# Optimization experiments

Hardware: AMD Instinct MI355X
Metric: run time of the kernel (lower is better)

Reference implementation:

```python
import jax, jax.numpy as jnp
import numpy as np

N = 100000       # n_entities + n_users
E = 1000000      # edges
D = 64           # entity_dim (phase/mod half-width)
R = 40           # n_relations
PI = 3.1415926235897933
GAMMA = 12.0
EMB_RANGE = (GAMMA + 2.0) / D   # (gamma + epsilon) / entity_dim
DIMS = [128, 64, 32, 16]        # conv_dim_list = [2*D] + [64,32,16]


def setup_inputs() -> dict:
    key = jax.random.key(0)
    ks = jax.random.split(key, 20)
    inp = {}
    inp["entity_embed"] = jax.random.uniform(ks[0], (N, 2 * D), minval=-EMB_RANGE, maxval=EMB_RANGE, dtype=jnp.float32)
    inp["rel_embed"] = jax.random.uniform(ks[1], (R, 3 * D), minval=-EMB_RANGE, maxval=EMB_RANGE, dtype=jnp.float32)
    inp["phase_w"] = jnp.array([[0.5 * EMB_RANGE]], dtype=jnp.float32)
    inp["mod_w"] = jnp.array([[1.0]], dtype=jnp.float32)
    names = [("W1_0", "b1_0", "W2_0", "b2_0"), ("W1_1", "b1_1", "W2_1", "b2_1"), ("W1_2", "b1_2", "W1_2b", "b2_2")]
    for i, (w1n, b1n, w2n, b2n) in enumerate(names):
        din, dout = DIMS[i], DIMS[i + 1]
        s = 1.0 / np.sqrt(din)
        inp[w1n] = jax.random.uniform(ks[2 + 4 * i], (dout, din), minval=-s, maxval=s, dtype=jnp.float32)
        inp[b1n] = jax.random.uniform(ks[3 + 4 * i], (dout,), minval=-s, maxval=s, dtype=jnp.float32)
        inp[w2n] = jax.random.uniform(ks[4 + 4 * i], (dout, din), minval=-s, maxval=s, dtype=jnp.float32)
        inp[b2n] = jax.random.uniform(ks[5 + 4 * i], (dout,), minval=-s, maxval=s, dtype=jnp.float32)
    inp["src"] = jax.random.randint(ks[14], (E,), 0, N, dtype=jnp.int32)
    inp["dst"] = jax.random.randint(ks[15], (E,), 0, N, dtype=jnp.int32)
    inp["etype"] = jax.random.randint(ks[16], (E,), 0, R, dtype=jnp.int32)
    return inp


def _edge_att(entity_embed, rel_embed, phase_w, mod_w, src, dst, etype):
    # HAKE att_score: h = dst node, t = src node (per original code)
    h = entity_embed[dst]            # [E, 2D]
    t = entity_embed[src]            # [E, 2D]
    r = rel_embed[etype]             # [E, 3D]
    scale = EMB_RANGE / PI
    ph, mh = h[:, :D], h[:, D:]
    pr, mr, br = r[:, :D], r[:, D:2 * D], r[:, 2 * D:]
    pt, mt = t[:, :D], t[:, D:]
    mr = jnp.abs(mr)
    br = jnp.minimum(br, 1.0)
    br = jnp.where(br < -mr, -mr, br)  # conditional write bias_relation[indicator] = -mod_relation
    mod_score = jnp.linalg.norm(mh * (mr + br) - mt * (1.0 - br), axis=1) * mod_w[0, 0]
    phase = (ph + pr - pt) / scale
    phase_score = jnp.sum(jnp.abs(jnp.sin(phase / 2.0)), axis=1) * phase_w[0, 0]
    att = phase_score + mod_score    # [E]
    # edge softmax over incoming edges of each dst node
    amax = jax.ops.segment_max(att, dst, num_segments=N)
    ex = jnp.exp(att - amax[dst])
    den = jax.ops.segment_sum(ex, dst, num_segments=N)
    return ex / den[dst]


def reference(entity_embed, rel_embed, phase_w, mod_w,
              W1_0, b1_0, W2_0, b2_0,
              W1_1, b1_1, W2_1, b2_1,
              W1_2, b1_2, W1_2b, b2_2,
              src, dst, etype):
    att = _edge_att(entity_embed, rel_embed, phase_w, mod_w, src, dst, etype)

    def layer(node, W1, b1, W2, b2):
        # u_mul_e('node','att','side') + sum('side','N_h')
        msg = node[src] * att[:, None]                    # [E, din]
        Nh = jax.ops.segment_sum(msg, dst, num_segments=N)
        # bi-interaction aggregator
        o = jax.nn.leaky_relu((node + Nh) @ W1.T + b1) + jax.nn.leaky_relu((node * Nh) @ W2.T + b2)
        nrm = jnp.linalg.norm(o, axis=1, keepdims=True)
        return o, o / jnp.maximum(nrm, 1e-12)             # (ego_embed, F.normalize)

    ego = entity_embed
    outs = [ego]
    for (W1, b1, W2, b2) in [(W1_0, b1_0, W2_0, b2_0), (W1_1, b1_1, W2_1, b2_1), (W1_2, b1_2, W1_2b, b2_2)]:
        ego, normed = layer(ego, W1, b1, W2, b2)
        outs.append(normed)
    return jnp.concatenate(outs, axis=1)                   # [N, 128+64+32+16]
```

## Files before the change

### kernel.cpp

```cpp
#include <hip/hip_runtime.h>
#include <math.h>


__global__ void hist_kernel(const int* __restrict__ dst, int* __restrict__ cnt,
                            int nedges) {
    int e = blockIdx.x * blockDim.x + threadIdx.x;
    if (e < nedges) atomicAdd(&cnt[dst[e]], 1);
}

__global__ __launch_bounds__(1024) void scan_block_kernel(
    const int* __restrict__ cnt, int* __restrict__ rowptr,
    int* __restrict__ bsum, int n) {
    __shared__ int swv[16];
    int tid = threadIdx.x, lane = tid & 63, wid = tid >> 6;
    int i = blockIdx.x * 1024 + tid;
    int v = (i < n) ? cnt[i] : 0;
    #pragma unroll
    for (int off = 1; off < 64; off <<= 1) {
        int t = __shfl_up(v, off, 64);
        if (lane >= off) v += t;
    }
    if (lane == 63) swv[wid] = v;
    __syncthreads();
    if (wid == 0) {
        int s = (lane < 16) ? swv[lane] : 0;
        #pragma unroll
        for (int off = 1; off < 16; off <<= 1) {
            int t = __shfl_up(s, off, 64);
            if (lane >= off) s += t;
        }
        if (lane < 16) swv[lane] = s;
    }
    __syncthreads();
    int offv = wid ? swv[wid - 1] : 0;
    if (i < n) rowptr[i + 1] = v + offv;
    if (tid == 1023) bsum[blockIdx.x] = v + offv;
}

__global__ __launch_bounds__(64) void scan_tops_kernel(
    const int* __restrict__ bsum, int* __restrict__ boff, int nb) {
    int l = threadIdx.x;
    int a = (2 * l < nb) ? bsum[2 * l] : 0;
    int b = (2 * l + 1 < nb) ? bsum[2 * l + 1] : 0;
    int s = a + b;
    #pragma unroll
    for (int off = 1; off < 64; off <<= 1) {
        int t = __shfl_up(s, off, 64);
        if (l >= off) s += t;
    }
    int excl = s - (a + b);
    if (2 * l < nb) boff[2 * l] = excl;
    if (2 * l + 1 < nb) boff[2 * l + 1] = excl + a;
}

__global__ __launch_bounds__(1024) void scan_add_kernel(
    int* __restrict__ rowptr, const int* __restrict__ boff, int n) {
    int i = blockIdx.x * 1024 + threadIdx.x;
    if (i < n) rowptr[i + 1] += boff[blockIdx.x];
    if (i == 0) rowptr[0] = 0;
}

__global__ void fill_kernel(const int* __restrict__ src, const int* __restrict__ dst,
                            const int* __restrict__ etype,
                            const int* __restrict__ rowptr, int* __restrict__ cursor,
                            int* __restrict__ se_s, int nedges) {
    int e = blockIdx.x * blockDim.x + threadIdx.x;
    if (e >= nedges) return;
    int d = dst[e];
    int slot = rowptr[d] + atomicAdd(&cursor[d], 1);
    se_s[slot] = src[e] | (etype[e] << 17);
}

__global__ void rel_prep_kernel(const float* __restrict__ rel,
                                float* __restrict__ relp, int nrel) {
    int i = blockIdx.x * blockDim.x + threadIdx.x;
    if (i >= nrel * 64) return;
    int r = i >> 6, d = i & 63;
    float pr = rel[r * 192 + d];
    float mr = fabsf(rel[r * 192 + 64 + d]);
    float br = rel[r * 192 + 128 + d];
    br = fminf(br, 1.0f);
    br = fmaxf(br, -mr);
    relp[r * 192 + d]       = mr + br;
    relp[r * 192 + 64 + d]  = 1.0f - br;
    relp[r * 192 + 128 + d] = pr;
}

__global__ __launch_bounds__(256) void att_gather_kernel(
    const float* __restrict__ embed, const float* __restrict__ relp,
    const float* __restrict__ pw, const float* __restrict__ mw,
    const int* __restrict__ se_s, const int* __restrict__ rowptr,
    float* __restrict__ att_s, float* __restrict__ ai,
    float* __restrict__ Nh, int nnodes)
{
    int v = blockIdx.x * 4 + (threadIdx.x >> 6);
    if (v >= nnodes) return;
    int lane = threadIdx.x & 63;
    int g = lane >> 3;
    int q = lane & 7;
    int beg = rowptr[v];
    int deg = rowptr[v + 1] - beg;

    const float K = (float)(0.5 * 3.1415926235897933 / 0.21875);
    float mwv = mw[0], pwv = pw[0];

    const float* hrow = embed + (size_t)v * 128;
    float4 hp0 = *(const float4*)(hrow + 8 * q);
    float4 hp1 = *(const float4*)(hrow + 8 * q + 4);
    float4 hm0 = *(const float4*)(hrow + 64 + 8 * q);
    float4 hm1 = *(const float4*)(hrow + 64 + 8 * q + 4);

    float den = 0.0f;
    float4 ap0 = make_float4(0.f, 0.f, 0.f, 0.f);
    float4 ap1 = make_float4(0.f, 0.f, 0.f, 0.f);
    float4 am0 = make_float4(0.f, 0.f, 0.f, 0.f);
    float4 am1 = make_float4(0.f, 0.f, 0.f, 0.f);

    for (int k0 = 0; k0 < deg; k0 += 8) {
        int ke = k0 + g;
        bool valid = ke < deg;
        int kc = beg + (valid ? ke : 0);
        int se = se_s[kc];
        int sidx = se & 0x1FFFF;
        int r = se >> 17;
        const float* trow = embed + (size_t)sidx * 128;
        float4 tp0 = *(const float4*)(trow + 8 * q);
        float4 tp1 = *(const float4*)(trow + 8 * q + 4);
        float4 tm0 = *(const float4*)(trow + 64 + 8 * q);
        float4 tm1 = *(const float4*)(trow + 64 + 8 * q + 4);
        const float* rrow = relp + r * 192;
        float4 A0 = *(const float4*)(rrow + 8 * q);
        float4 A1 = *(const float4*)(rrow + 8 * q + 4);
        float4 B0 = *(const float4*)(rrow + 64 + 8 * q);
        float4 B1 = *(const float4*)(rrow + 64 + 8 * q + 4);
        float4 P0 = *(const float4*)(rrow + 128 + 8 * q);
        float4 P1 = *(const float4*)(rrow + 128 + 8 * q + 4);

        float pp;
        pp  = fabsf(__sinf((hp0.x + P0.x - tp0.x) * K));
        pp += fabsf(__sinf((hp0.y + P0.y - tp0.y) * K));
        pp += fabsf(__sinf((hp0.z + P0.z - tp0.z) * K));
        pp += fabsf(__sinf((hp0.w + P0.w - tp0.w) * K));
        pp += fabsf(__sinf((hp1.x + P1.x - tp1.x) * K));
        pp += fabsf(__sinf((hp1.y + P1.y - tp1.y) * K));
        pp += fabsf(__sinf((hp1.z + P1.z - tp1.z) * K));
        pp += fabsf(__sinf((hp1.w + P1.w - tp1.w) * K));

        float d0 = hm0.x * A0.x - tm0.x * B0.x;
        float d1 = hm0.y * A0.y - tm0.y * B0.y;
        float d2 = hm0.z * A0.z - tm0.z * B0.z;
        float d3 = hm0.w * A0.w - tm0.w * B0.w;
        float d4 = hm1.x * A1.x - tm1.x * B1.x;
        float d5 = hm1.y * A1.y - tm1.y * B1.y;
        float d6 = hm1.z * A1.z - tm1.z * B1.z;
        float d7 = hm1.w * A1.w - tm1.w * B1.w;
        float qq = ((d0 * d0 + d1 * d1) + (d2 * d2 + d3 * d3)) +
                   ((d4 * d4 + d5 * d5) + (d6 * d6 + d7 * d7));

        #pragma unroll
        for (int off = 1; off < 8; off <<= 1) {
            pp += __shfl_xor(pp, off, 64);
            qq += __shfl_xor(qq, off, 64);
        }
        float s = sqrtf(qq) * mwv + pp * pwv;
        float w = valid ? __expf(s) : 0.0f;
        den += w;
        ap0.x = fmaf(w, tp0.x, ap0.x); ap0.y = fmaf(w, tp0.y, ap0.y);
        ap0.z = fmaf(w, tp0.z, ap0.z); ap0.w = fmaf(w, tp0.w, ap0.w);
        ap1.x = fmaf(w, tp1.x, ap1.x); ap1.y = fmaf(w, tp1.y, ap1.y);
        ap1.z = fmaf(w, tp1.z, ap1.z); ap1.w = fmaf(w, tp1.w, ap1.w);
        am0.x = fmaf(w, tm0.x, am0.x); am0.y = fmaf(w, tm0.y, am0.y);
        am0.z = fmaf(w, tm0.z, am0.z); am0.w = fmaf(w, tm0.w, am0.w);
        am1.x = fmaf(w, tm1.x, am1.x); am1.y = fmaf(w, tm1.y, am1.y);
        am1.z = fmaf(w, tm1.z, am1.z); am1.w = fmaf(w, tm1.w, am1.w);
        if (valid && q == 0) att_s[kc] = w;
    }

    #pragma unroll
    for (int off = 8; off < 64; off <<= 1) {
        ap0.x += __shfl_xor(ap0.x, off, 64); ap0.y += __shfl_xor(ap0.y, off, 64);
        ap0.z += __shfl_xor(ap0.z, off, 64); ap0.w += __shfl_xor(ap0.w, off, 64);
        ap1.x += __shfl_xor(ap1.x, off, 64); ap1.y += __shfl_xor(ap1.y, off, 64);
        ap1.z += __shfl_xor(ap1.z, off, 64); ap1.w += __shfl_xor(ap1.w, off, 64);
        am0.x += __shfl_xor(am0.x, off, 64); am0.y += __shfl_xor(am0.y, off, 64);
        am0.z += __shfl_xor(am0.z, off, 64); am0.w += __shfl_xor(am0.w, off, 64);
        am1.x += __shfl_xor(am1.x, off, 64); am1.y += __shfl_xor(am1.y, off, 64);
        am1.z += __shfl_xor(am1.z, off, 64); am1.w += __shfl_xor(am1.w, off, 64);
        den += __shfl_xor(den, off, 64);
    }
    float invd = (deg > 0) ? 1.0f / den : 0.0f;
    if (g == 0) {
        float* pn = Nh + (size_t)v * 128;
        *(float4*)(pn + 8 * q) = make_float4(ap0.x * invd, ap0.y * invd,
                                             ap0.z * invd, ap0.w * invd);
        *(float4*)(pn + 8 * q + 4) = make_float4(ap1.x * invd, ap1.y * invd,
                                                 ap1.z * invd, ap1.w * invd);
        *(float4*)(pn + 64 + 8 * q) = make_float4(am0.x * invd, am0.y * invd,
                                                  am0.z * invd, am0.w * invd);
        *(float4*)(pn + 64 + 8 * q + 4) = make_float4(am1.x * invd, am1.y * invd,
                                                      am1.z * invd, am1.w * invd);
        if (q == 0) ai[v] = invd;
    }
}

template<int DIN>
__global__ __launch_bounds__(256) void gather_kernel(
    const float* __restrict__ node, int nstride, const float* __restrict__ nrm,
    const float* __restrict__ att_s, const int* __restrict__ se_s,
    const int* __restrict__ rowptr, const float* __restrict__ ai,
    float* __restrict__ Nh, int nnodes)
{
    constexpr int LPE = DIN / 4;
    constexpr int EP  = 64 / LPE;
    constexpr int U   = 4;
    int v = blockIdx.x * 4 + (threadIdx.x >> 6);
    if (v >= nnodes) return;
    int lane = threadIdx.x & 63;
    int sub = lane / LPE;
    int c = lane % LPE;
    int beg = rowptr[v];
    int deg = rowptr[v + 1] - beg;

    float4 acc = make_float4(0.f, 0.f, 0.f, 0.f);
    for (int kb = 0; kb < deg; kb += 64) {
        int kc = kb + lane;
        bool inr = kc < deg;
        int sv = inr ? (se_s[beg + kc] & 0x1FFFF) : 0;
        float av = inr ? att_s[beg + kc] * nrm[sv] : 0.0f;
        int kmax = min(64, deg - kb);
        for (int k0 = 0; k0 < kmax; k0 += U * EP) {
            float a[U];
            const float4* p[U];
            #pragma unroll
            for (int u = 0; u < U; ++u) {
                int kk = k0 + u * EP + sub;
                bool val = kk < kmax;
                int kidx = val ? kk : 0;
                int ssrc = __shfl(sv, kidx, 64);
                float aa = __shfl(av, kidx, 64);
                a[u] = val ? aa : 0.0f;
                p[u] = (const float4*)(node + (size_t)ssrc * nstride + 4 * c);
            }
            float4 rv[U];
            #pragma unroll
            for (int u = 0; u < U; ++u) rv[u] = *p[u];
            #pragma unroll
            for (int u = 0; u < U; ++u) {
                acc.x += a[u] * rv[u].x;
                acc.y += a[u] * rv[u].y;
                acc.z += a[u] * rv[u].z;
                acc.w += a[u] * rv[u].w;
            }
        }
    }
    #pragma unroll
    for (int off = LPE; off < 64; off <<= 1) {
        acc.x += __shfl_xor(acc.x, off, 64);
        acc.y += __shfl_xor(acc.y, off, 64);
        acc.z += __shfl_xor(acc.z, off, 64);
        acc.w += __shfl_xor(acc.w, off, 64);
    }
    if (sub == 0) {
        float aiv = ai[v];
        float4 o = make_float4(acc.x * aiv, acc.y * aiv,
                               acc.z * aiv, acc.w * aiv);
        *(float4*)(Nh + (size_t)v * DIN + 4 * c) = o;
    }
}

template<int DIN, int DOUT, bool NRM, bool EGO>
__global__ __launch_bounds__(512) void gemm_kernel(
    const float* __restrict__ node, int nstride, const float* __restrict__ nrm_in,
    const float* __restrict__ Nh,
    const float* __restrict__ W1, const float* __restrict__ b1,
    const float* __restrict__ W2, const float* __restrict__ b2,
    float* __restrict__ out, int out_col, float* __restrict__ nrm_out, int nnodes)
{
    constexpr int XS = DIN + 1;
    constexpr int DH = DOUT / 8;
    __shared__ float sx1[64 * XS], sx2[64 * XS];
    __shared__ float sred[8][64];

    int tid = threadIdx.x;
    int tile0 = blockIdx.x * 64;

    for (int idx = tid; idx < 64 * (DIN / 4); idx += 512) {
        int row = idx / (DIN / 4), c = idx % (DIN / 4);
        int v = tile0 + row;
        float4 nv4 = make_float4(0.f, 0.f, 0.f, 0.f);
        float4 hv4 = make_float4(0.f, 0.f, 0.f, 0.f);
        if (v < nnodes) {
            nv4 = *(const float4*)(node + (size_t)v * nstride + 4 * c);
            hv4 = *(const float4*)(Nh + (size_t)v * DIN + 4 * c);
            if (EGO)
                *(float4*)(out + (size_t)v * 240 + 4 * c) = nv4;
            if (NRM) {
                float rn = nrm_in[v];
                nv4.x *= rn; nv4.y *= rn; nv4.z *= rn; nv4.w *= rn;
            }
        }
        float* p1 = sx1 + row * XS + 4 * c;
        float* p2 = sx2 + row * XS + 4 * c;
        p1[0] = nv4.x + hv4.x; p1[1] = nv4.y + hv4.y;
        p1[2] = nv4.z + hv4.z; p1[3] = nv4.w + hv4.w;
        p2[0] = nv4.x * hv4.x; p2[1] = nv4.y * hv4.y;
        p2[2] = nv4.z * hv4.z; p2[3] = nv4.w * hv4.w;
    }
    __syncthreads();

    int lane = tid & 63;
    int jh = __builtin_amdgcn_readfirstlane(tid >> 6);
    int j0 = jh * DH;
    int v = tile0 + lane;
    bool act = v < nnodes;

    float acc1[DH], acc2[DH];
    #pragma unroll
    for (int j = 0; j < DH; ++j) { acc1[j] = 0.f; acc2[j] = 0.f; }

    const float* px1 = sx1 + lane * XS;
    const float* px2 = sx2 + lane * XS;
    #pragma unroll 1
    for (int ic = 0; ic < DIN; ic += 8) {
        float x1c[8], x2c[8];
        #pragma unroll
        for (int t = 0; t < 8; ++t) {
            x1c[t] = px1[ic + t];
            x2c[t] = px2[ic + t];
        }
        #pragma unroll
        for (int j = 0; j < DH; ++j) {
            const float* w1 = W1 + (size_t)(j0 + j) * DIN + ic;
            const float* w2 = W2 + (size_t)(j0 + j) * DIN + ic;
            #pragma unroll
            for (int t = 0; t < 8; ++t) {
                acc1[j] = fmaf(x1c[t], w1[t], acc1[j]);
                acc2[j] = fmaf(x2c[t], w2[t], acc2[j]);
            }
        }
    }

    float o[DH];
    float ss = 0.0f;
    #pragma unroll
    for (int j = 0; j < DH; ++j) {
        float a1 = acc1[j] + b1[j0 + j];
        a1 = a1 >= 0.0f ? a1 : 0.01f * a1;
        float a2 = acc2[j] + b2[j0 + j];
        a2 = a2 >= 0.0f ? a2 : 0.01f * a2;
        o[j] = a1 + a2;
        ss += o[j] * o[j];
    }
    sred[jh][lane] = ss;
    __syncthreads();
    float tot = 0.0f;
    #pragma unroll
    for (int q = 0; q < 8; ++q) tot += sred[q][lane];
    float nv2 = fmaxf(sqrtf(tot), 1e-12f);
    float inv = 1.0f / nv2;
    if (act) {
        float* po = out + (size_t)v * 240 + out_col + j0;
        if (DH >= 4) {
            #pragma unroll
            for (int j = 0; j < DH; j += 4) {
                float4 st = make_float4(o[j] * inv, o[j + 1] * inv,
                                        o[j + 2] * inv, o[j + 3] * inv);
                *(float4*)(po + j) = st;
            }
        } else {
            #pragma unroll
            for (int j = 0; j < DH; ++j) po[j] = o[j] * inv;
        }
        if (nrm_out && jh == 0) nrm_out[v] = nv2;
    }
}

extern "C" void kernel_launch(void* const* d_in, const int* in_sizes, int n_in,
                              void* d_out, int out_size, void* d_ws, size_t ws_size,
                              hipStream_t stream) {
    const float* embed = (const float*)d_in[0];
    const float* rel   = (const float*)d_in[1];
    const float* pw    = (const float*)d_in[2];
    const float* mw    = (const float*)d_in[3];
    const float* W1_0  = (const float*)d_in[4];
    const float* b1_0  = (const float*)d_in[5];
    const float* W2_0  = (const float*)d_in[6];
    const float* b2_0  = (const float*)d_in[7];
    const float* W1_1  = (const float*)d_in[8];
    const float* b1_1  = (const float*)d_in[9];
    const float* W2_1  = (const float*)d_in[10];
    const float* b2_1  = (const float*)d_in[11];
    const float* W1_2  = (const float*)d_in[12];
    const float* b1_2  = (const float*)d_in[13];
    const float* W1_2b = (const float*)d_in[14];
    const float* b2_2  = (const float*)d_in[15];
    const int* src   = (const int*)d_in[16];
    const int* dst   = (const int*)d_in[17];
    const int* etype = (const int*)d_in[18];
    float* out = (float*)d_out;

    const int n = in_sizes[0] / 128;
    const int e = in_sizes[16];
    const int r = in_sizes[1] / 192;

    char* ws = (char*)d_ws;
    float* att_s  = (float*)ws;
    int*   se_s   = (int*)(att_s + e);
    float* Nh     = (float*)(se_s + e);
    int*   rowptr = (int*)(Nh + (size_t)n * 128);
    int*   cnt    = rowptr + n + 1;
    int*   cursor = cnt + n;
    int*   bsum   = cursor + n;
    int*   boff   = bsum + 128;
    float* nrm1   = (float*)(boff + 128);
    float* nrm2   = nrm1 + n;
    float* relp   = nrm2 + n;
    float* ai     = relp + r * 192;

    const int NB = (n + 1023) / 1024;

    hipMemsetAsync(cnt, 0, (size_t)(2 * n) * 4, stream);
    hist_kernel<<<(e + 255) / 256, 256, 0, stream>>>(dst, cnt, e);
    scan_block_kernel<<<NB, 1024, 0, stream>>>(cnt, rowptr, bsum, n);
    scan_tops_kernel<<<1, 64, 0, stream>>>(bsum, boff, NB);
    scan_add_kernel<<<NB, 1024, 0, stream>>>(rowptr, boff, n);
    fill_kernel<<<(e + 255) / 256, 256, 0, stream>>>(src, dst, etype, rowptr,
                                                     cursor, se_s, e);
    rel_prep_kernel<<<(r * 64 + 255) / 256, 256, 0, stream>>>(rel, relp, r);

    int gblocks = (n + 3) / 4;
    int tiles = (n + 63) / 64;

    att_gather_kernel<<<gblocks, 256, 0, stream>>>(
        embed, relp, pw, mw, se_s, rowptr, att_s, ai, Nh, n);

    gemm_kernel<128, 64, false, true><<<tiles, 512, 0, stream>>>(
        embed, 128, nullptr, Nh, W1_0, b1_0, W2_0, b2_0, out, 128, nrm1, n);
    gather_kernel<64><<<gblocks, 256, 0, stream>>>(
        out + 128, 240, nrm1, att_s, se_s, rowptr, ai, Nh, n);
    gemm_kernel<64, 32, true, false><<<tiles, 512, 0, stream>>>(
        out + 128, 240, nrm1, Nh, W1_1, b1_1, W2_1, b2_1, out, 192, nrm2, n);
    gather_kernel<32><<<gblocks, 256, 0, stream>>>(
        out + 192, 240, nrm2, att_s, se_s, rowptr, ai, Nh, n);
    gemm_kernel<32, 16, true, false><<<tiles, 512, 0, stream>>>(
        out + 192, 240, nrm2, Nh, W1_2, b1_2, W1_2b, b2_2, out, 224, nullptr, n);
}
```

Measured before the change: 471.9 us.

## Persistent attention gather with shared-memory relation table and batched edge loads

Folds the relation preprocessing into the attention-gather kernel, which now builds the clamped relation table in shared memory once per block, and drops the separate rel_prep launch. The kernel becomes persistent (1024 blocks of 512 threads striding over nodes). Each wave now uses 16 lanes per edge and 4 edges per step instead of 8 lanes and 8 edges. Each wave loads up to 64 packed edge indices with one coalesced read and broadcasts them by shuffle. This trades some edge-level parallelism and extra shuffles for fewer global loads of relation rows and edge indices, plus one fewer launch. The shared table is sized for exactly 40 relations.

Measured after the change: 490.2 us. 3.9% more time.

```diff
diff --git a/kernel.cpp b/kernel.cpp
--- a/kernel.cpp
+++ b/kernel.cpp
@@ -71,135 +71,114 @@
     se_s[slot] = src[e] | (etype[e] << 17);
 }
 
-__global__ void rel_prep_kernel(const float* __restrict__ rel,
-                                float* __restrict__ relp, int nrel) {
-    int i = blockIdx.x * blockDim.x + threadIdx.x;
-    if (i >= nrel * 64) return;
-    int r = i >> 6, d = i & 63;
-    float pr = rel[r * 192 + d];
-    float mr = fabsf(rel[r * 192 + 64 + d]);
-    float br = rel[r * 192 + 128 + d];
-    br = fminf(br, 1.0f);
-    br = fmaxf(br, -mr);
-    relp[r * 192 + d]       = mr + br;
-    relp[r * 192 + 64 + d]  = 1.0f - br;
-    relp[r * 192 + 128 + d] = pr;
-}
-
-__global__ __launch_bounds__(256) void att_gather_kernel(
-    const float* __restrict__ embed, const float* __restrict__ relp,
+__global__ __launch_bounds__(512) void att_gather_kernel(
+    const float* __restrict__ embed, const float* __restrict__ rel,
     const float* __restrict__ pw, const float* __restrict__ mw,
     const int* __restrict__ se_s, const int* __restrict__ rowptr,
     float* __restrict__ att_s, float* __restrict__ ai,
-    float* __restrict__ Nh, int nnodes)
+    float* __restrict__ Nh, int nnodes, int nrel)
 {
-    int v = blockIdx.x * 4 + (threadIdx.x >> 6);
-    if (v >= nnodes) return;
-    int lane = threadIdx.x & 63;
-    int g = lane >> 3;
-    int q = lane & 7;
-    int beg = rowptr[v];
-    int deg = rowptr[v + 1] - beg;
+    __shared__ float sRel[40 * 196];
+    int tid = threadIdx.x;
+
+    for (int idx = tid; idx < nrel * 64; idx += 512) {
+        int r = idx >> 6, d = idx & 63;
+        float pr = rel[r * 192 + d];
+        float mr = fabsf(rel[r * 192 + 64 + d]);
+        float br = rel[r * 192 + 128 + d];
+        br = fminf(br, 1.0f);
+        br = fmaxf(br, -mr);
+        sRel[r * 196 + d]       = mr + br;
+        sRel[r * 196 + 64 + d]  = 1.0f - br;
+        sRel[r * 196 + 128 + d] = pr;
+    }
+    __syncthreads();
 
     const float K = (float)(0.5 * 3.1415926235897933 / 0.21875);
     float mwv = mw[0], pwv = pw[0];
 
-    const float* hrow = embed + (size_t)v * 128;
-    float4 hp0 = *(const float4*)(hrow + 8 * q);
-    float4 hp1 = *(const float4*)(hrow + 8 * q + 4);
-    float4 hm0 = *(const float4*)(hrow + 64 + 8 * q);
-    float4 hm1 = *(const float4*)(hrow + 64 + 8 * q + 4);
-
-    float den = 0.0f;
-    float4 ap0 = make_float4(0.f, 0.f, 0.f, 0.f);
-    float4 ap1 = make_float4(0.f, 0.f, 0.f, 0.f);
-    float4 am0 = make_float4(0.f, 0.f, 0.f, 0.f);
-    float4 am1 = make_float4(0.f, 0.f, 0.f, 0.f);
-
-    for (int k0 = 0; k0 < deg; k0 += 8) {
-        int ke = k0 + g;
-        bool valid = ke < deg;
-        int kc = beg + (valid ? ke : 0);
-        int se = se_s[kc];
-        int sidx = se & 0x1FFFF;
-        int r = se >> 17;
-        const float* trow = embed + (size_t)sidx * 128;
-        float4 tp0 = *(const float4*)(trow + 8 * q);
-        float4 tp1 = *(const float4*)(trow + 8 * q + 4);
-        float4 tm0 = *(const float4*)(trow + 64 + 8 * q);
-        float4 tm1 = *(const float4*)(trow + 64 + 8 * q + 4);
-        const float* rrow = relp + r * 192;
-        float4 A0 = *(const float4*)(rrow + 8 * q);
-        float4 A1 = *(const float4*)(rrow + 8 * q + 4);
-        float4 B0 = *(const float4*)(rrow + 64 + 8 * q);
-        float4 B1 = *(const float4*)(rrow + 64 + 8 * q + 4);
-        float4 P0 = *(const float4*)(rrow + 128 + 8 * q);
-        float4 P1 = *(const float4*)(rrow + 128 + 8 * q + 4);
-
-        float pp;
-        pp  = fabsf(__sinf((hp0.x + P0.x - tp0.x) * K));
-        pp += fabsf(__sinf((hp0.y + P0.y - tp0.y) * K));
-        pp += fabsf(__sinf((hp0.z + P0.z - tp0.z) * K));
-        pp += fabsf(__sinf((hp0.w + P0.w - tp0.w) * K));
-        pp += fabsf(__sinf((hp1.x + P1.x - tp1.x) * K));
-        pp += fabsf(__sinf((hp1.y + P1.y - tp1.y) * K));
-        pp += fabsf(__sinf((hp1.z + P1.z - tp1.z) * K));
-        pp += fabsf(__sinf((hp1.w + P1.w - tp1.w) * K));
-
-        float d0 = hm0.x * A0.x - tm0.x * B0.x;
-        float d1 = hm0.y * A0.y - tm0.y * B0.y;
-        float d2 = hm0.z * A0.z - tm0.z * B0.z;
-        float d3 = hm0.w * A0.w - tm0.w * B0.w;
-        float d4 = hm1.x * A1.x - tm1.x * B1.x;
-        float d5 = hm1.y * A1.y - tm1.y * B1.y;
-        float d6 = hm1.z * A1.z - tm1.z * B1.z;
-        float d7 = hm1.w * A1.w - tm1.w * B1.w;
-        float qq = ((d0 * d0 + d1 * d1) + (d2 * d2 + d3 * d3)) +
-                   ((d4 * d4 + d5 * d5) + (d6 * d6 + d7 * d7));
+    int wave = tid >> 6, lane = tid & 63;
+    int g = lane >> 4;
+    int q = lane & 15;
+
+    for (int v = blockIdx.x * 8 + wave; v < nnodes; v += gridDim.x * 8) {
+        int beg = rowptr[v];
+        int deg = rowptr[v + 1] - beg;
+
+        const float* hrow = embed + (size_t)v * 128;
+        float4 hp = *(const float4*)(hrow + 4 * q);
+        float4 hm = *(const float4*)(hrow + 64 + 4 * q);
+
+        float den = 0.0f;
+        float4 accp = make_float4(0.f, 0.f, 0.f, 0.f);
+        float4 accm = make_float4(0.f, 0.f, 0.f, 0.f);
+
+        for (int kb = 0; kb < deg; kb += 64) {
+            int kchunk = min(64, deg - kb);
+            int sev = (lane < kchunk) ? se_s[beg + kb + lane] : 0;
+            for (int k0 = 0; k0 < kchunk; k0 += 4) {
+                int ke = k0 + g;
+                bool valid = ke < kchunk;
+                int se = __shfl(sev, valid ? ke : 0, 64);
+                int sidx = se & 0x1FFFF;
+                int r = se >> 17;
+                const float* trow = embed + (size_t)sidx * 128;
+                float4 tp = *(const float4*)(trow + 4 * q);
+                float4 tm = *(const float4*)(trow + 64 + 4 * q);
+                const float* rrow = sRel + r * 196;
+                float4 A4 = *(const float4*)(rrow + 4 * q);
+                float4 B4 = *(const float4*)(rrow + 64 + 4 * q);
+                float4 P4 = *(const float4*)(rrow + 128 + 4 * q);
+
+                float pp;
+                pp  = fabsf(__sinf((hp.x + P4.x - tp.x) * K));
+                pp += fabsf(__sinf((hp.y + P4.y - tp.y) * K));
+                pp += fabsf(__sinf((hp.z + P4.z - tp.z) * K));
+                pp += fabsf(__sinf((hp.w + P4.w - tp.w) * K));
+
+                float d0 = hm.x * A4.x - tm.x * B4.x;
+                float d1 = hm.y * A4.y - tm.y * B4.y;
+                float d2 = hm.z * A4.z - tm.z * B4.z;
+                float d3 = hm.w * A4.w - tm.w * B4.w;
+                float qq = (d0 * d0 + d1 * d1) + (d2 * d2 + d3 * d3);
+
+                #pragma unroll
+                for (int off = 1; off < 16; off <<= 1) {
+                    pp += __shfl_xor(pp, off, 64);
+                    qq += __shfl_xor(qq, off, 64);
+                }
+                float s = sqrtf(qq) * mwv + pp * pwv;
+                float w = valid ? __expf(s) : 0.0f;
+                den += w;
+                accp.x = fmaf(w, tp.x, accp.x); accp.y = fmaf(w, tp.y, accp.y);
+                accp.z = fmaf(w, tp.z, accp.z); accp.w = fmaf(w, tp.w, accp.w);
+                accm.x = fmaf(w, tm.x, accm.x); accm.y = fmaf(w, tm.y, accm.y);
+                accm.z = fmaf(w, tm.z, accm.z); accm.w = fmaf(w, tm.w, accm.w);
+                if (valid && q == 0) att_s[beg + kb + ke] = w;
+            }
+        }
 
         #pragma unroll
-        for (int off = 1; off < 8; off <<= 1) {
-            pp += __shfl_xor(pp, off, 64);
-            qq += __shfl_xor(qq, off, 64);
-        }
-        float s = sqrtf(qq) * mwv + pp * pwv;
-        float w = valid ? __expf(s) : 0.0f;
-        den += w;
-        ap0.x = fmaf(w, tp0.x, ap0.x); ap0.y = fmaf(w, tp0.y, ap0.y);
-        ap0.z = fmaf(w, tp0.z, ap0.z); ap0.w = fmaf(w, tp0.w, ap0.w);
-        ap1.x = fmaf(w, tp1.x, ap1.x); ap1.y = fmaf(w, tp1.y, ap1.y);
-        ap1.z = fmaf(w, tp1.z, ap1.z); ap1.w = fmaf(w, tp1.w, ap1.w);
-        am0.x = fmaf(w, tm0.x, am0.x); am0.y = fmaf(w, tm0.y, am0.y);
-        am0.z = fmaf(w, tm0.z, am0.z); am0.w = fmaf(w, tm0.w, am0.w);
-        am1.x = fmaf(w, tm1.x, am1.x); am1.y = fmaf(w, tm1.y, am1.y);
-        am1.z = fmaf(w, tm1.z, am1.z); am1.w = fmaf(w, tm1.w, am1.w);
-        if (valid && q == 0) att_s[kc] = w;
-    }
-
-    #pragma unroll
-    for (int off = 8; off < 64; off <<= 1) {
-        ap0.x += __shfl_xor(ap0.x, off, 64); ap0.y += __shfl_xor(ap0.y, off, 64);
-        ap0.z += __shfl_xor(ap0.z, off, 64); ap0.w += __shfl_xor(ap0.w, off, 64);
-        ap1.x += __shfl_xor(ap1.x, off, 64); ap1.y += __shfl_xor(ap1.y, off, 64);
-        ap1.z += __shfl_xor(ap1.z, off, 64); ap1.w += __shfl_xor(ap1.w, off, 64);
-        am0.x += __shfl_xor(am0.x, off, 64); am0.y += __shfl_xor(am0.y, off, 64);
-        am0.z += __shfl_xor(am0.z, off, 64); am0.w += __shfl_xor(am0.w, off, 64);
-        am1.x += __shfl_xor(am1.x, off, 64); am1.y += __shfl_xor(am1.y, off, 64);
-        am1.z += __shfl_xor(am1.z, off, 64); am1.w += __shfl_xor(am1.w, off, 64);
-        den += __shfl_xor(den, off, 64);
-    }
-    float invd = (deg > 0) ? 1.0f / den : 0.0f;
-    if (g == 0) {
-        float* pn = Nh + (size_t)v * 128;
-        *(float4*)(pn + 8 * q) = make_float4(ap0.x * invd, ap0.y * invd,
-                                             ap0.z * invd, ap0.w * invd);
-        *(float4*)(pn + 8 * q + 4) = make_float4(ap1.x * invd, ap1.y * invd,
-                                                 ap1.z * invd, ap1.w * invd);
-        *(float4*)(pn + 64 + 8 * q) = make_float4(am0.x * invd, am0.y * invd,
-                                                  am0.z * invd, am0.w * invd);
-        *(float4*)(pn + 64 + 8 * q + 4) = make_float4(am1.x * invd, am1.y * invd,
-                                                      am1.z * invd, am1.w * invd);
-        if (q == 0) ai[v] = invd;
+        for (int off = 16; off < 64; off <<= 1) {
+            accp.x += __shfl_xor(accp.x, off, 64);
+            accp.y += __shfl_xor(accp.y, off, 64);
+            accp.z += __shfl_xor(accp.z, off, 64);
+            accp.w += __shfl_xor(accp.w, off, 64);
+            accm.x += __shfl_xor(accm.x, off, 64);
+            accm.y += __shfl_xor(accm.y, off, 64);
+            accm.z += __shfl_xor(accm.z, off, 64);
+            accm.w += __shfl_xor(accm.w, off, 64);
+            den += __shfl_xor(den, off, 64);
+        }
+        float invd = (deg > 0) ? 1.0f / den : 0.0f;
+        if (g == 0) {
+            float* pn = Nh + (size_t)v * 128;
+            *(float4*)(pn + 4 * q) = make_float4(accp.x * invd, accp.y * invd,
+                                                 accp.z * invd, accp.w * invd);
+            *(float4*)(pn + 64 + 4 * q) = make_float4(accm.x * invd, accm.y * invd,
+                                                      accm.z * invd, accm.w * invd);
+            if (q == 0) ai[v] = invd;
+        }
     }
 }
 
@@ -414,8 +393,7 @@
     int*   boff   = bsum + 128;
     float* nrm1   = (float*)(boff + 128);
     float* nrm2   = nrm1 + n;
-    float* relp   = nrm2 + n;
-    float* ai     = relp + r * 192;
+    float* ai     = nrm2 + n;
 
     const int NB = (n + 1023) / 1024;
 
@@ -426,13 +404,12 @@
     scan_add_kernel<<<NB, 1024, 0, stream>>>(rowptr, boff, n);
     fill_kernel<<<(e + 255) / 256, 256, 0, stream>>>(src, dst, etype, rowptr,
                                                      cursor, se_s, e);
-    rel_prep_kernel<<<(r * 64 + 255) / 256, 256, 0, stream>>>(rel, relp, r);
 
     int gblocks = (n + 3) / 4;
     int tiles = (n + 63) / 64;
 
-    att_gather_kernel<<<gblocks, 256, 0, stream>>>(
-        embed, relp, pw, mw, se_s, rowptr, att_s, ai, Nh, n);
+    att_gather_kernel<<<1024, 512, 0, stream>>>(
+        embed, rel, pw, mw, se_s, rowptr, att_s, ai, Nh, n, r);
 
     gemm_kernel<128, 64, false, true><<<tiles, 512, 0, stream>>>(
         embed, 128, nullptr, Nh, W1_0, b1_0, W2_0, b2_0, out, 128, nrm1, n);
```
